# Optimization experiments

Measured on AMD Instinct MI355X. Metric: run time of the kernel, lower is better.

## Reference

```python
import jax, jax.numpy as jnp
import numpy as np

N_SAMPLES = 16384
IN_FEATURES = 2048
N_COMPONENTS = 512
MAX_CROSS_TERMS = 512
# With n_components=512, max_cross_terms=512: interaction_depth=2 -> only pairwise
# cross terms, and n_pairwise = min(512*511//2, 512) = 512 (the first 512 pairs in
# lexicographic (i, j), i<j order -- exactly what the chunked torch loops produce).
_pi, _pj = np.triu_indices(N_COMPONENTS, k=1)  # lexicographic row-major order
PAIR_I = jnp.asarray(_pi[:MAX_CROSS_TERMS])
PAIR_J = jnp.asarray(_pj[:MAX_CROSS_TERMS])
SQRT_EPS = 1e-8


def setup_inputs() -> dict:
    key = jax.random.key(0)
    k1, k2 = jax.random.split(key)
    X = jax.random.normal(k1, (N_SAMPLES, IN_FEATURES), dtype=jnp.float32)
    projection = jax.random.normal(k2, (IN_FEATURES, N_COMPONENTS), dtype=jnp.float32) / np.sqrt(N_COMPONENTS)
    return {"X": X, "projection": projection}


def reference(X, projection):
    # Random projection: [N, in] @ [in, C] -> [N, C]
    Xp = X @ projection
    n = X.shape[0]
    bias = jnp.ones((n, 1), dtype=X.dtype)                 # 'bias' chunk
    p1 = Xp                                                # power_1
    p2 = Xp * Xp                                           # power_2
    p3 = p2 * Xp                                           # power_3
    pairs = Xp[:, PAIR_I] * Xp[:, PAIR_J]                  # pairwise cross terms
    sq = jnp.sqrt(jnp.abs(Xp) + SQRT_EPS)                  # sqrt features
    # Feature layout matches torch offsets: bias | p1 | p2 | p3 | cross | sqrt
    return jnp.concatenate([bias, p1, p2, p3, pairs, sq], axis=1)  # [N, 2561]
```

## Files before the change

kernel.cpp:

```cpp
#include <hip/hip_runtime.h>
#include <hip/hip_bf16.h>
#include <math.h>


typedef __attribute__((ext_vector_type(4))) float f32x4;
typedef __attribute__((ext_vector_type(8))) short bf16x8;

#define MM 16384
#define NN 512
#define KK 2048
#define OUTW 2561

#define BM 64
#define BN 128
#define BK 32
#define NT (KK / BK)

__device__ __forceinline__ short f2bf(float x) {
  union { __hip_bfloat16 b; short s; } u;
  u.b = __float2bfloat16(x);
  return u.s;
}

__device__ __forceinline__ bf16x8 cvt8(f32x4 a, f32x4 b) {
  bf16x8 r;
  r[0] = f2bf(a[0]); r[1] = f2bf(a[1]); r[2] = f2bf(a[2]); r[3] = f2bf(a[3]);
  r[4] = f2bf(b[0]); r[5] = f2bf(b[1]); r[6] = f2bf(b[2]); r[7] = f2bf(b[3]);
  return r;
}

__device__ __forceinline__ void gl_lds16(const void* g, void* l) {
  __builtin_amdgcn_global_load_lds((const __attribute__((address_space(1))) unsigned int*)g,
                                   (__attribute__((address_space(3))) unsigned int*)l, 16, 0, 0);
}

__global__ __launch_bounds__(256) void prep_b(const float* __restrict__ P, short* __restrict__ Bt) {
  __shared__ float ts[64][65];
  const int tid = threadIdx.x;
  const int k0 = (blockIdx.x >> 3) * 64;
  const int n0 = (blockIdx.x & 7) * 64;
#pragma unroll
  for (int j = 0; j < 16; ++j) {
    int idx = j * 256 + tid;
    int kr = idx >> 6, nc = idx & 63;
    ts[kr][nc] = P[(size_t)(k0 + kr) * NN + n0 + nc];
  }
  __syncthreads();
#pragma unroll
  for (int j = 0; j < 16; ++j) {
    int idx = j * 256 + tid;
    int nr = idx >> 6, kc = idx & 63;
    Bt[(size_t)(n0 + nr) * KK + k0 + kc] = f2bf(ts[kc][nr]);
  }
}

__global__ __launch_bounds__(256) void gemm3(const float* __restrict__ X,
                                             const short* __restrict__ Bt,
                                             float* __restrict__ out) {
  __shared__ short As[2][BM * BK];
  __shared__ short Bs[2][BN * BK];

  const int tid = threadIdx.x;
  const int wid = tid >> 6, lane = tid & 63;
  const int lrow = lane & 15, kh = lane >> 4;
  const int wr = wid >> 1, wc = wid & 1;

  const int bid = blockIdx.x;
  const int tile = (bid & 7) * 128 + (bid >> 3);
  const int m0 = (tile >> 2) * BM;
  const int n0 = (tile & 3) * BN;

  const int arow = tid >> 2, akq = tid & 3;
  const float* aG = X + (size_t)(m0 + arow) * KK + akq * 8;
  const int aoff = arow * 32 + ((akq ^ ((arow >> 1) & 3)) << 3);

  const int kd = (lane & 3) ^ ((lane >> 3) & 3);
  const short* bG[2];
  int bOff[2];
#pragma unroll
  for (int p = 0; p < 2; ++p) {
    int R0 = (p * 4 + wid) * 16;
    bOff[p] = R0 * 32;
    bG[p] = Bt + (size_t)(n0 + R0 + (lane >> 2)) * KK + kd * 8;
  }

  f32x4 acc[2][4];
#pragma unroll
  for (int m = 0; m < 2; ++m)
#pragma unroll
    for (int n = 0; n < 4; ++n) acc[m][n] = (f32x4)0.0f;

#pragma unroll
  for (int p = 0; p < 2; ++p) gl_lds16(bG[p], &Bs[0][bOff[p]]);
  f32x4 a0 = *(const f32x4*)aG;
  f32x4 a1 = *(const f32x4*)(aG + 4);
  *(bf16x8*)&As[0][aoff] = cvt8(a0, a1);
  a0 = *(const f32x4*)(aG + BK);
  a1 = *(const f32x4*)(aG + BK + 4);
  __syncthreads();

  int cur = 0;
  for (int t = 0; t < NT; ++t) {
    if (t + 1 < NT) {
#pragma unroll
      for (int p = 0; p < 2; ++p) gl_lds16(bG[p] + (size_t)(t + 1) * BK, &Bs[cur ^ 1][bOff[p]]);
      *(bf16x8*)&As[cur ^ 1][aoff] = cvt8(a0, a1);
      int t2 = (t + 2 < NT) ? t + 2 : t;
      a0 = *(const f32x4*)(aG + (size_t)t2 * BK);
      a1 = *(const f32x4*)(aG + (size_t)t2 * BK + 4);
    }
    const int sw = ((lrow >> 1) & 3);
    bf16x8 af[2], bfr[4];
#pragma unroll
    for (int m = 0; m < 2; ++m) {
      int r = wr * 32 + m * 16 + lrow;
      af[m] = *(const bf16x8*)&As[cur][r * 32 + ((kh ^ sw) << 3)];
    }
#pragma unroll
    for (int n = 0; n < 4; ++n) {
      int r = wc * 64 + n * 16 + lrow;
      bfr[n] = *(const bf16x8*)&Bs[cur][r * 32 + ((kh ^ sw) << 3)];
    }
#pragma unroll
    for (int m = 0; m < 2; ++m)
#pragma unroll
      for (int n = 0; n < 4; ++n)
        acc[m][n] = __builtin_amdgcn_mfma_f32_16x16x32_bf16(af[m], bfr[n], acc[m][n], 0, 0, 0);
    __syncthreads();
    cur ^= 1;
  }

#pragma unroll
  for (int m = 0; m < 2; ++m)
#pragma unroll
    for (int n = 0; n < 4; ++n)
#pragma unroll
      for (int r = 0; r < 4; ++r) {
        int row = m0 + wr * 32 + m * 16 + kh * 4 + r;
        int col = n0 + wc * 64 + n * 16 + lrow;
        out[(size_t)row * OUTW + 1 + col] = acc[m][n][r];
      }
}

__global__ __launch_bounds__(512) void epi_k(float* __restrict__ out) {
  const int r = blockIdx.x;
  const int c = threadIdx.x;
  float* row = out + (size_t)r * OUTW;
  __shared__ float s[NN];
  float xp = row[1 + c];
  s[c] = xp;
  __syncthreads();
  float p2 = xp * xp;
  float p3 = p2 * xp;
  float sq = sqrtf(fabsf(xp) + 1e-8f);
  float pr = (c < 511) ? s[0] * s[c + 1] : s[1] * s[2];
  if (c == 0) row[0] = 1.0f;
  row[513 + c] = p2;
  row[1025 + c] = p3;
  row[1537 + c] = pr;
  row[2049 + c] = sq;
}

#define FBM 128
#define FBN 128
#define FPAD 40

__global__ __launch_bounds__(256) void gemm_k(const float* __restrict__ A,
                                              const float* __restrict__ B,
                                              float* __restrict__ out) {
  __shared__ __align__(16) short Asf[FBM][FPAD];
  __shared__ __align__(16) short Bsf[FBN][FPAD];
  const int tid = threadIdx.x;
  const int bx = blockIdx.x;
  const int m0 = (bx >> 2) * FBM;
  const int n0 = (bx & 3) * FBN;
  const int wid = tid >> 6, lane = tid & 63;
  const int wr = wid >> 1, wc = wid & 1;
  const int lrow = lane & 15, kh = lane >> 4;
  f32x4 acc[4][4];
#pragma unroll
  for (int i = 0; i < 4; i++)
#pragma unroll
    for (int j = 0; j < 4; j++) acc[i][j] = (f32x4)0.0f;
  for (int k0 = 0; k0 < KK; k0 += BK) {
#pragma unroll
    for (int i = 0; i < 4; i++) {
      int fid = i * 256 + tid;
      int ar = fid >> 3, ac = (fid & 7) << 2;
      f32x4 v = *(const f32x4*)(A + (size_t)(m0 + ar) * KK + (k0 + ac));
      short h0 = f2bf(v[0]), h1 = f2bf(v[1]), h2 = f2bf(v[2]), h3 = f2bf(v[3]);
      Asf[ar][ac] = h0; Asf[ar][ac + 1] = h1; Asf[ar][ac + 2] = h2; Asf[ar][ac + 3] = h3;
    }
#pragma unroll
    for (int i = 0; i < 4; i++) {
      int fid = i * 256 + tid;
      int br = fid >> 5, bc = (fid & 31) << 2;
      f32x4 v = *(const f32x4*)(B + (size_t)(k0 + br) * NN + (n0 + bc));
#pragma unroll
      for (int j = 0; j < 4; j++) Bsf[bc + j][br] = f2bf(v[j]);
    }
    __syncthreads();
    bf16x8 af[4], bf[4];
#pragma unroll
    for (int m = 0; m < 4; m++) af[m] = *(const bf16x8*)&Asf[wr * 64 + m * 16 + lrow][kh * 8];
#pragma unroll
    for (int n = 0; n < 4; n++) bf[n] = *(const bf16x8*)&Bsf[wc * 64 + n * 16 + lrow][kh * 8];
#pragma unroll
    for (int m = 0; m < 4; m++)
#pragma unroll
      for (int n = 0; n < 4; n++)
        acc[m][n] = __builtin_amdgcn_mfma_f32_16x16x32_bf16(af[m], bf[n], acc[m][n], 0, 0, 0);
    __syncthreads();
  }
#pragma unroll
  for (int m = 0; m < 4; m++)
#pragma unroll
    for (int n = 0; n < 4; n++)
#pragma unroll
      for (int r = 0; r < 4; r++) {
        int row = m0 + wr * 64 + m * 16 + kh * 4 + r;
        int col = n0 + wc * 64 + n * 16 + lrow;
        out[(size_t)row * OUTW + 1 + col] = acc[m][n][r];
      }
}

extern "C" void kernel_launch(void* const* d_in, const int* in_sizes, int n_in,
                              void* d_out, int out_size, void* d_ws, size_t ws_size,
                              hipStream_t stream) {
  const float* X = (const float*)d_in[0];
  const float* P = (const float*)d_in[1];
  float* out = (float*)d_out;
  (void)in_sizes; (void)n_in; (void)out_size;

  if (ws_size >= (size_t)NN * KK * sizeof(short)) {
    short* Bt = (short*)d_ws;
    prep_b<<<dim3(256), dim3(256), 0, stream>>>(P, Bt);
    gemm3<<<dim3((MM / BM) * (NN / BN)), dim3(256), 0, stream>>>(X, Bt, out);
  } else {
    gemm_k<<<dim3(512), dim3(256), 0, stream>>>(X, P, out);
  }
  epi_k<<<dim3(MM), dim3(512), 0, stream>>>(out);
}
```

Measured before the change: 138.5 us.

## Replace LDS-tiled GEMM with register-direct full-width tile GEMM

Replaces the LDS double-buffered 64x128 GEMM with a 512-thread kernel where each block computes a 64x512 row strip and each wave loads its A and B MFMA fragments straight from global memory into registers. There is no LDS and no barriers, and loads are software-pipelined two k-steps ahead. Because each block covers all 512 columns, X is read exactly once instead of four times. In exchange, each lane does strided 16-byte global loads with no reuse across waves, so B traffic through L2 grows, and register pressure rises to 2x8 accumulators plus double-buffered fragments.

```diff
diff --git a/kernel.cpp b/kernel.cpp
--- a/kernel.cpp
+++ b/kernel.cpp
@@ -11,8 +11,7 @@
 #define KK 2048
 #define OUTW 2561
 
-#define BM 64
-#define BN 128
+#define BM7 64
 #define BK 32
 #define NT (KK / BK)
 
@@ -29,11 +28,6 @@
   return r;
 }
 
-__device__ __forceinline__ void gl_lds16(const void* g, void* l) {
-  __builtin_amdgcn_global_load_lds((const __attribute__((address_space(1))) unsigned int*)g,
-                                   (__attribute__((address_space(3))) unsigned int*)l, 16, 0, 0);
-}
-
 __global__ __launch_bounds__(256) void prep_b(const float* __restrict__ P, short* __restrict__ Bt) {
   __shared__ float ts[64][65];
   const int tid = threadIdx.x;
@@ -54,90 +48,86 @@
   }
 }
 
-__global__ __launch_bounds__(256) void gemm3(const float* __restrict__ X,
-                                             const short* __restrict__ Bt,
-                                             float* __restrict__ out) {
-  __shared__ short As[2][BM * BK];
-  __shared__ short Bs[2][BN * BK];
-
+__global__ __launch_bounds__(512, 2) void gemm7(const float* __restrict__ X,
+                                                const short* __restrict__ Bt,
+                                                float* __restrict__ out) {
   const int tid = threadIdx.x;
   const int wid = tid >> 6, lane = tid & 63;
   const int lrow = lane & 15, kh = lane >> 4;
-  const int wr = wid >> 1, wc = wid & 1;
-
-  const int bid = blockIdx.x;
-  const int tile = (bid & 7) * 128 + (bid >> 3);
-  const int m0 = (tile >> 2) * BM;
-  const int n0 = (tile & 3) * BN;
-
-  const int arow = tid >> 2, akq = tid & 3;
-  const float* aG = X + (size_t)(m0 + arow) * KK + akq * 8;
-  const int aoff = arow * 32 + ((akq ^ ((arow >> 1) & 3)) << 3);
-
-  const int kd = (lane & 3) ^ ((lane >> 3) & 3);
-  const short* bG[2];
-  int bOff[2];
-#pragma unroll
-  for (int p = 0; p < 2; ++p) {
-    int R0 = (p * 4 + wid) * 16;
-    bOff[p] = R0 * 32;
-    bG[p] = Bt + (size_t)(n0 + R0 + (lane >> 2)) * KK + kd * 8;
-  }
-
-  f32x4 acc[2][4];
+  const int wr = wid >> 2, wc = wid & 3;
+
+  const int m0 = blockIdx.x * BM7;
+
+  const float* aP0 = X + (size_t)(m0 + wr * 32 + lrow) * KK + kh * 8;
+  const float* aP1 = aP0 + (size_t)16 * KK;
+  const short* bP[8];
+#pragma unroll
+  for (int n = 0; n < 8; ++n)
+    bP[n] = Bt + (size_t)(wc * 128 + n * 16 + lrow) * KK + kh * 8;
+
+  f32x4 acc[2][8];
 #pragma unroll
   for (int m = 0; m < 2; ++m)
 #pragma unroll
-    for (int n = 0; n < 4; ++n) acc[m][n] = (f32x4)0.0f;
-
-#pragma unroll
-  for (int p = 0; p < 2; ++p) gl_lds16(bG[p], &Bs[0][bOff[p]]);
-  f32x4 a0 = *(const f32x4*)aG;
-  f32x4 a1 = *(const f32x4*)(aG + 4);
-  *(bf16x8*)&As[0][aoff] = cvt8(a0, a1);
-  a0 = *(const f32x4*)(aG + BK);
-  a1 = *(const f32x4*)(aG + BK + 4);
-  __syncthreads();
-
-  int cur = 0;
-  for (int t = 0; t < NT; ++t) {
-    if (t + 1 < NT) {
-#pragma unroll
-      for (int p = 0; p < 2; ++p) gl_lds16(bG[p] + (size_t)(t + 1) * BK, &Bs[cur ^ 1][bOff[p]]);
-      *(bf16x8*)&As[cur ^ 1][aoff] = cvt8(a0, a1);
-      int t2 = (t + 2 < NT) ? t + 2 : t;
-      a0 = *(const f32x4*)(aG + (size_t)t2 * BK);
-      a1 = *(const f32x4*)(aG + (size_t)t2 * BK + 4);
-    }
-    const int sw = ((lrow >> 1) & 3);
-    bf16x8 af[2], bfr[4];
-#pragma unroll
-    for (int m = 0; m < 2; ++m) {
-      int r = wr * 32 + m * 16 + lrow;
-      af[m] = *(const bf16x8*)&As[cur][r * 32 + ((kh ^ sw) << 3)];
-    }
-#pragma unroll
-    for (int n = 0; n < 4; ++n) {
-      int r = wc * 64 + n * 16 + lrow;
-      bfr[n] = *(const bf16x8*)&Bs[cur][r * 32 + ((kh ^ sw) << 3)];
-    }
-#pragma unroll
-    for (int m = 0; m < 2; ++m)
-#pragma unroll
-      for (int n = 0; n < 4; ++n)
-        acc[m][n] = __builtin_amdgcn_mfma_f32_16x16x32_bf16(af[m], bfr[n], acc[m][n], 0, 0, 0);
-    __syncthreads();
-    cur ^= 1;
+    for (int n = 0; n < 8; ++n) acc[m][n] = (f32x4)0.0f;
+
+  f32x4 a0m0l, a0m0h, a0m1l, a0m1h;
+  f32x4 a1m0l, a1m0h, a1m1l, a1m1h;
+  bf16x8 b0[8], b1[8];
+
+  a0m0l = *(const f32x4*)(aP0);      a0m0h = *(const f32x4*)(aP0 + 4);
+  a0m1l = *(const f32x4*)(aP1);      a0m1h = *(const f32x4*)(aP1 + 4);
+  a1m0l = *(const f32x4*)(aP0 + BK); a1m0h = *(const f32x4*)(aP0 + BK + 4);
+  a1m1l = *(const f32x4*)(aP1 + BK); a1m1h = *(const f32x4*)(aP1 + BK + 4);
+#pragma unroll
+  for (int n = 0; n < 8; ++n) b0[n] = *(const bf16x8*)(bP[n]);
+
+  for (int t = 0; t < NT; t += 2) {
+    {
+#pragma unroll
+      for (int n = 0; n < 8; ++n) b1[n] = *(const bf16x8*)(bP[n] + (size_t)(t + 1) * BK);
+      bf16x8 af0 = cvt8(a0m0l, a0m0h);
+      bf16x8 af1 = cvt8(a0m1l, a0m1h);
+      {
+        size_t toff = (size_t)((t + 2 < NT) ? t + 2 : NT - 1) * BK;
+        a0m0l = *(const f32x4*)(aP0 + toff); a0m0h = *(const f32x4*)(aP0 + toff + 4);
+        a0m1l = *(const f32x4*)(aP1 + toff); a0m1h = *(const f32x4*)(aP1 + toff + 4);
+      }
+#pragma unroll
+      for (int n = 0; n < 8; ++n)
+        acc[0][n] = __builtin_amdgcn_mfma_f32_16x16x32_bf16(af0, b0[n], acc[0][n], 0, 0, 0);
+#pragma unroll
+      for (int n = 0; n < 8; ++n)
+        acc[1][n] = __builtin_amdgcn_mfma_f32_16x16x32_bf16(af1, b0[n], acc[1][n], 0, 0, 0);
+    }
+    {
+      size_t bo = (size_t)((t + 2 < NT) ? t + 2 : NT - 1) * BK;
+#pragma unroll
+      for (int n = 0; n < 8; ++n) b0[n] = *(const bf16x8*)(bP[n] + bo);
+      bf16x8 af0 = cvt8(a1m0l, a1m0h);
+      bf16x8 af1 = cvt8(a1m1l, a1m1h);
+      {
+        size_t toff = (size_t)((t + 3 < NT) ? t + 3 : NT - 1) * BK;
+        a1m0l = *(const f32x4*)(aP0 + toff); a1m0h = *(const f32x4*)(aP0 + toff + 4);
+        a1m1l = *(const f32x4*)(aP1 + toff); a1m1h = *(const f32x4*)(aP1 + toff + 4);
+      }
+#pragma unroll
+      for (int n = 0; n < 8; ++n)
+        acc[0][n] = __builtin_amdgcn_mfma_f32_16x16x32_bf16(af0, b1[n], acc[0][n], 0, 0, 0);
+#pragma unroll
+      for (int n = 0; n < 8; ++n)
+        acc[1][n] = __builtin_amdgcn_mfma_f32_16x16x32_bf16(af1, b1[n], acc[1][n], 0, 0, 0);
+    }
   }
 
 #pragma unroll
   for (int m = 0; m < 2; ++m)
 #pragma unroll
-    for (int n = 0; n < 4; ++n)
+    for (int n = 0; n < 8; ++n)
 #pragma unroll
       for (int r = 0; r < 4; ++r) {
         int row = m0 + wr * 32 + m * 16 + kh * 4 + r;
-        int col = n0 + wc * 64 + n * 16 + lrow;
+        int col = wc * 128 + n * 16 + lrow;
         out[(size_t)row * OUTW + 1 + col] = acc[m][n][r];
       }
 }
@@ -235,7 +225,7 @@
   if (ws_size >= (size_t)NN * KK * sizeof(short)) {
     short* Bt = (short*)d_ws;
     prep_b<<<dim3(256), dim3(256), 0, stream>>>(P, Bt);
-    gemm3<<<dim3((MM / BM) * (NN / BN)), dim3(256), 0, stream>>>(X, Bt, out);
+    gemm7<<<dim3(MM / BM7), dim3(512), 0, stream>>>(X, Bt, out);
   } else {
     gemm_k<<<dim3(512), dim3(256), 0, stream>>>(X, P, out);
   }
```

New measurement: 221.1 us. +59.6%, slower.
